# Performance work log

Measured on AMD Instinct MI355X. Metric: run time of the kernel, lower is better.

Reference implementation:

```python
import jax, jax.numpy as jnp
import numpy as np

H = 4          # num_heads
K_HOP = 2
EPS = 1e-5


def _ln(x, g, b):
    m = jnp.mean(x, axis=-1, keepdims=True)
    v = jnp.mean((x - m) ** 2, axis=-1, keepdims=True)
    return (x - m) * jax.lax.rsqrt(v + EPS) * g + b


def setup_inputs() -> dict:
    key = jax.random.key(0)
    B, T, N, D = 16, 24, 512, 64
    F = 256
    ks = jax.random.split(key, 16)
    s = 0.02
    inp = {
        'x': jax.random.normal(ks[0], (B, T, N, D), dtype=jnp.float32),
        'adj': jax.random.uniform(ks[1], (N, N), dtype=jnp.float32),
        'Wq': jax.random.normal(ks[2], (D, D), dtype=jnp.float32) * s,
        'bq': jnp.zeros((D,), jnp.float32),
        'Wk': jax.random.normal(ks[3], (D, D), dtype=jnp.float32) * s,
        'bk': jnp.zeros((D,), jnp.float32),
        'Wv': jax.random.normal(ks[4], (D, D), dtype=jnp.float32) * s,
        'bv': jnp.zeros((D,), jnp.float32),
        'Wo': jax.random.normal(ks[5], (D, D), dtype=jnp.float32) * s,
        'bo': jnp.zeros((D,), jnp.float32),
        'gcW': jax.random.normal(ks[6], (K_HOP + 1, D, D), dtype=jnp.float32) * s,
        'gcb': jnp.zeros((K_HOP + 1, D), jnp.float32),
        'W1': jax.random.normal(ks[7], (D, F), dtype=jnp.float32) * s,
        'b1': jnp.zeros((F,), jnp.float32),
        'W2': jax.random.normal(ks[8], (F, D), dtype=jnp.float32) * s,
        'b2': jnp.zeros((D,), jnp.float32),
        'g_t': jnp.ones((D,), jnp.float32), 'b_t': jnp.zeros((D,), jnp.float32),
        'g_g': jnp.ones((D,), jnp.float32), 'b_g': jnp.zeros((D,), jnp.float32),
        'g_f': jnp.ones((D,), jnp.float32), 'b_f': jnp.zeros((D,), jnp.float32),
    }
    return inp


def _forward(x, adj, Wq, bq, Wk, bk, Wv, bv, Wo, bo, gcW, gcb,
             W1, b1, W2, b2, g_t, b_t, g_g, b_g, g_f, b_f):
    B, T, N, D = x.shape
    hd = D // H
    scale = hd ** -0.5

    # ---- temporal multi-head attention (per node, along T) ----
    def heads(y):
        return y.reshape(B, T, N, H, hd)
    q = heads(x @ Wq + bq)
    k = heads(x @ Wk + bk)
    v = heads(x @ Wv + bv)
    scores = jnp.einsum('bqnhd,bknhd->bnhqk', q, k) * scale  # [B,N,H,T,T]
    attn = jax.nn.softmax(scores, axis=-1)
    att = jnp.einsum('bnhqk,bknhd->bqnhd', attn, v).reshape(B, T, N, D)
    att = att @ Wo + bo
    h = _ln(x + att, g_t, b_t)

    # ---- K-hop graph convolution: sum_k A_hat^k X W_k ----
    A = adj + jnp.eye(N, dtype=adj.dtype)
    deg = A.sum(-1)
    dinv = jnp.clip(deg, 1e-12, None) ** -0.5
    Ahat = dinv[:, None] * A * dinv[None, :]  # [N,N], shared across B*T
    prop = h
    gout = prop @ gcW[0] + gcb[0]
    for kk in range(1, K_HOP + 1):
        prop = jnp.einsum('mn,btnd->btmd', Ahat, prop)
        gout = gout + prop @ gcW[kk] + gcb[kk]
    h = _ln(h + gout, g_g, b_g)

    # ---- FFN (exact GELU, as torch default) ----
    f = jax.nn.gelu(h @ W1 + b1, approximate=False) @ W2 + b2
    return _ln(h + f, g_f, b_f)


def reference(x, adj, Wq, bq, Wk, bk, Wv, bv, Wo, bo, gcW, gcb,
              W1, b1, W2, b2, g_t, b_t, g_g, b_g, g_f, b_f):
    return _forward(x, adj, Wq, bq, Wk, bk, Wv, bv, Wo, bo, gcW, gcb,
                    W1, b1, W2, b2, g_t, b_t, g_g, b_g, g_f, b_f)
```

## Files before the change

kernel.cpp:

```cpp
#include <hip/hip_runtime.h>
#include <hip/hip_bf16.h>
#include <math.h>

typedef __hip_bfloat16 bf16;
typedef unsigned short ushort_t;

__device__ __forceinline__ float us2f(ushort_t u){
  union { unsigned u; float f; } v; v.u = ((unsigned)u) << 16; return v.f;
}
__device__ __forceinline__ ushort_t f2us(float f){
  union { __bf16 b; ushort_t u; } v; v.b = (__bf16)f; return v.u;
}

__device__ __forceinline__ float gelu_f(float x){
  float y = x * fmaf(0.0356774081f, x*x, 0.7978845608f);
  float e = __expf(-2.0f*y);
  return x * __builtin_amdgcn_rcpf(1.0f + e);
}

#define B_ 16
#define T_ 24
#define N_ 512
#define D_ 64
#define F_ 256

typedef __attribute__((ext_vector_type(8)))  short  frag8;
typedef __attribute__((ext_vector_type(16))) float  accv16;

__device__ __forceinline__ float wave_sum(float v){
#pragma unroll
  for (int off = 32; off > 0; off >>= 1) v += __shfl_xor(v, off, 64);
  return v;
}

__global__ __launch_bounds__(64) void k_dinv(const float* __restrict__ adj,
                                             float* __restrict__ dinv){
  int m = blockIdx.x;
  float s = 0.f;
  for (int n = threadIdx.x; n < N_; n += 64) s += adj[m*N_ + n];
  s = wave_sum(s);
  if (threadIdx.x == 0){
    float deg = s + 1.0f;
    dinv[m] = rsqrtf(fmaxf(deg, 1e-12f));
  }
}

__global__ __launch_bounds__(256) void k_ahat(const float* __restrict__ adj,
                                              const float* __restrict__ dinv,
                                              ushort_t* __restrict__ AhatB,
                                              ushort_t* __restrict__ AhatBT){
  int idx = blockIdx.x*256 + threadIdx.x;
  int m = idx >> 9, n = idx & (N_-1);
  float a = adj[idx] + (m == n ? 1.f : 0.f);
  ushort_t v = f2us(dinv[m]*a*dinv[n]);
  AhatB[idx] = v;
  AhatBT[n*N_ + m] = v;
}

__global__ __launch_bounds__(256, 4) void k_ah2(
    const ushort_t* __restrict__ A1,
    const ushort_t* __restrict__ A1T,
    ushort_t* __restrict__ A2)
{
  __shared__ __align__(16) ushort_t Ab[64][72];
  __shared__ __align__(16) ushort_t Bb[64][72];
  __shared__ __align__(16) ushort_t Yt[64][72];
  int tid  = threadIdx.x;
  int lane = tid & 63, w = tid >> 6;
  int mw = (w >> 1) * 32, nw = (w & 1) * 32;
  int l31 = lane & 31, lh = lane >> 5;
  int m0 = blockIdx.x * 64, n0 = blockIdx.y * 64;
  int ar = tid >> 3, ac8 = (tid & 7) * 8;

  accv16 acc = {};
  for (int k0 = 0; k0 < N_; k0 += 64){
#pragma unroll
    for (int g = 0; g < 2; g++){
      int rr = ar + g*32;
      *(uint4*)&Ab[rr][ac8] = *(const uint4*)&A1 [(size_t)(m0 + rr)*N_ + k0 + ac8];
      *(uint4*)&Bb[rr][ac8] = *(const uint4*)&A1T[(size_t)(n0 + rr)*N_ + k0 + ac8];
    }
    __syncthreads();
#pragma unroll
    for (int kk = 0; kk < 64; kk += 16){
      frag8 af = *(const frag8*)&Ab[mw + l31][kk + lh*8];
      frag8 bf = *(const frag8*)&Bb[nw + l31][kk + lh*8];
      acc = __builtin_amdgcn_mfma_f32_32x32x16_bf16(af, bf, acc, 0, 0, 0);
    }
    __syncthreads();
  }
#pragma unroll
  for (int r = 0; r < 16; r++){
    int row = mw + (r & 3) + 8*(r >> 2) + 4*lh;
    Yt[row][nw + l31] = f2us(acc[r]);
  }
  __syncthreads();
#pragma unroll
  for (int g = 0; g < 2; g++){
    int rr = ar + g*32;
    *(uint4*)&A2[(size_t)(m0 + rr)*N_ + n0 + ac8] = *(const uint4*)&Yt[rr][ac8];
  }
}

__global__ __launch_bounds__(256) void k_wprep(
    const float* __restrict__ W1, const float* __restrict__ W2,
    const float* __restrict__ Wq, const float* __restrict__ Wk,
    const float* __restrict__ Wv, const float* __restrict__ Wo,
    const float* __restrict__ gcW,
    ushort_t* __restrict__ W1t, ushort_t* __restrict__ W2t,
    ushort_t* __restrict__ Wqt, ushort_t* __restrict__ Wkt,
    ushort_t* __restrict__ Wvt, ushort_t* __restrict__ Wot,
    ushort_t* __restrict__ gWt){
  int o = blockIdx.x*256 + threadIdx.x;
  int f = o >> 6, e = o & 63;
  W1t[o] = f2us(W1[e*256 + f]);
  int d = o >> 8, e2 = o & 255;
  W2t[o] = f2us(W2[e2*64 + d]);
  if (o < 4096){
    int dd = o >> 6, ee = o & 63;
    Wqt[o] = f2us(Wq[ee*64 + dd]);
    Wkt[o] = f2us(Wk[ee*64 + dd]);
    Wvt[o] = f2us(Wv[ee*64 + dd]);
    Wot[o] = f2us(Wo[ee*64 + dd]);
    gWt[o]        = f2us(gcW[       ee*64 + dd]);
    gWt[4096 + o] = f2us(gcW[4096 + ee*64 + dd]);
    gWt[8192 + o] = f2us(gcW[8192 + ee*64 + dd]);
  }
}

__global__ __launch_bounds__(256, 4) void k_attn_m(
    const float* __restrict__ x,
    const ushort_t* __restrict__ Wqt, const float* __restrict__ bq,
    const ushort_t* __restrict__ Wkt, const float* __restrict__ bk,
    const ushort_t* __restrict__ Wvt, const float* __restrict__ bv,
    const ushort_t* __restrict__ Wot, const float* __restrict__ bo,
    const float* __restrict__ g_t, const float* __restrict__ b_t,
    float* __restrict__ h1)
{
  __shared__ __align__(16) char smem[28928];
  ushort_t (*xsA)[72] = (ushort_t(*)[72]) smem;
  ushort_t (*qs)[72]  = (ushort_t(*)[72])(smem + 6912);
  ushort_t (*ks)[72]  = (ushort_t(*)[72])(smem + 13824);
  float    (*Os)[65]  = (float(*)[65])   (smem + 6912);
  ushort_t *vsT       = (ushort_t*)(smem + 20736);

  int tid = threadIdx.x;
  int lane = tid & 63, w = tid >> 6;
  int l31 = lane & 31, lh = lane >> 5;
  int mt = (w >> 1) * 32, nt = (w & 1) * 32;
  int b = blockIdx.x >> 8;
  int n0 = (blockIdx.x & 255) * 2;

  {
    uint4 z4 = {0,0,0,0};
#pragma unroll
    for (int i = 0; i < 2; i++)
      *(uint4*)(smem + 20736 + (tid + i*256)*16) = z4;
  }
#pragma unroll
  for (int i = 0; i < 3; i++){
    int idx = tid + i*256;
    int row = idx >> 4, d4 = (idx & 15) * 4;
    int node = row >= 24;
    int t = row - node*24;
    const float4 v = *(const float4*)&x[(((size_t)b*T_ + t)*N_ + n0 + node)*D_ + d4];
    ushort_t tmp[4] = { f2us(v.x), f2us(v.y), f2us(v.z), f2us(v.w) };
    *(unsigned long long*)&xsA[row][d4] = *(unsigned long long*)tmp;
  }
  __syncthreads();

#pragma unroll
  for (int pj = 0; pj < 3; pj++){
    const ushort_t* Wp = (pj==0 ? Wqt : pj==1 ? Wkt : Wvt);
    accv16 a = {};
#pragma unroll
    for (int kk = 0; kk < 64; kk += 16){
      frag8 af = *(const frag8*)&xsA[mt + l31][kk + lh*8];
      frag8 bf = *(const frag8*)&Wp[(size_t)(nt + l31)*64 + kk + lh*8];
      a = __builtin_amdgcn_mfma_f32_32x32x16_bf16(af, bf, a, 0, 0, 0);
    }
    float bias = (pj==0 ? bq : pj==1 ? bk : bv)[nt + l31];
    if (pj < 2){
      ushort_t (*dst)[72] = (pj==0 ? qs : ks);
#pragma unroll
      for (int r = 0; r < 16; r++){
        int row = mt + (r & 3) + 8*(r >> 2) + 4*lh;
        if (row < 48) dst[row][nt + l31] = f2us(a[r] + bias);
      }
    } else {
      int cl = nt + l31;
#pragma unroll
      for (int r = 0; r < 16; r++){
        int row = mt + (r & 3) + 8*(r >> 2) + 4*lh;
        if (row < 48){
          int node = (row >= 24);
          int t2 = row - node*24;
          int Rr = node*64 + cl;
          vsT[Rr*32 + (((t2 >> 3) ^ ((Rr >> 1) & 3)) << 3) + (t2 & 7)] = f2us(a[r] + bias);
        }
      }
    }
  }
  __syncthreads();

  int vs_s = (l31 >> 1) & 3;
#pragma unroll
  for (int gi = 0; gi < 2; gi++){
    int g = w*2 + gi;
    int node = g >> 2, hh = g & 3;
    accv16 s = {};
    frag8 kf = *(const frag8*)&ks[node*24 + l31][hh*16 + lh*8];
    frag8 qf = *(const frag8*)&qs[node*24 + l31][hh*16 + lh*8];
    s = __builtin_amdgcn_mfma_f32_32x32x16_bf16(kf, qf, s, 0, 0, 0);
    float e[12]; float sm = 0.f;
#pragma unroll
    for (int r = 0; r < 12; r++){ e[r] = __expf(s[r]*0.25f); sm += e[r]; }
    sm += __shfl_xor(sm, 32, 64);
    float rinv = 1.0f / sm;
    union { unsigned long long q; ushort_t u[4]; } a0, a1, a2;
#pragma unroll
    for (int j = 0; j < 4; j++){
      a0.u[j] = f2us(e[j]   * rinv);
      a1.u[j] = f2us(e[4+j] * rinv);
      a2.u[j] = f2us(e[8+j] * rinv);
    }
    unsigned long long send1 = lh ? a0.q : a1.q;
    unsigned long long r1 = __shfl_xor(send1, 32, 64);
    unsigned long long r2 = __shfl_xor(a2.q, 32, 64);
    union { frag8 f; unsigned long long q[2]; } f0, f1;
    f0.q[0] = lh ? r1   : a0.q;
    f0.q[1] = lh ? a1.q : r1;
    f1.q[0] = lh ? 0ULL : a2.q;
    f1.q[1] = lh ? 0ULL : r2;
    int vrow = node*64 + hh*16 + (l31 & 15);
    const ushort_t* vb = &vsT[vrow*32];
    frag8 bf0 = *(const frag8*)&vb[((0 + lh) ^ vs_s) << 3];
    frag8 bf1 = *(const frag8*)&vb[((2 + lh) ^ vs_s) << 3];
    accv16 acc = {};
    acc = __builtin_amdgcn_mfma_f32_32x32x16_bf16(f0.f, bf0, acc, 0, 0, 0);
    acc = __builtin_amdgcn_mfma_f32_32x32x16_bf16(f1.f, bf1, acc, 0, 0, 0);
    if (l31 < 16){
#pragma unroll
      for (int r = 0; r < 12; r++){
        int row = (r & 3) + 8*(r >> 2) + 4*lh;
        xsA[node*24 + row][hh*16 + l31] = f2us(acc[r]);
      }
    }
  }
  __syncthreads();

  accv16 ao = {};
#pragma unroll
  for (int kk = 0; kk < 64; kk += 16){
    frag8 af = *(const frag8*)&xsA[mt + l31][kk + lh*8];
    frag8 bf = *(const frag8*)&Wot[(size_t)(nt + l31)*64 + kk + lh*8];
    ao = __builtin_amdgcn_mfma_f32_32x32x16_bf16(af, bf, ao, 0, 0, 0);
  }
  {
    float bov = bo[nt + l31];
#pragma unroll
    for (int r = 0; r < 16; r++){
      int row = mt + (r & 3) + 8*(r >> 2) + 4*lh;
      if (row < 48) Os[row][nt + l31] = ao[r] + bov;
    }
  }
  __syncthreads();
  {
    float gv = g_t[lane], bvv = b_t[lane];
#pragma unroll
    for (int i = 0; i < 12; i++){
      int row = w + i*4;
      int node = row >= 24;
      int t = row - node*24;
      size_t gaddr = (((size_t)b*T_ + t)*N_ + n0 + node)*D_ + lane;
      float v = Os[row][lane] + x[gaddr];
      float m = wave_sum(v) * (1.f/64.f);
      float df = v - m;
      float var = wave_sum(df*df) * (1.f/64.f);
      h1[gaddr] = df * rsqrtf(var + 1e-5f) * gv + bvv;
    }
  }
}

__global__ __launch_bounds__(256, 8) void k_hT(const float* __restrict__ h,
                                               ushort_t* __restrict__ hT){
  __shared__ __align__(16) ushort_t tb[64][76];
  int tid = threadIdx.x;
  int n0 = (blockIdx.x & 7) * 64;
  size_t bt = blockIdx.x >> 3;
  const float* src = h + (bt*N_ + n0)*D_;
#pragma unroll
  for (int i = 0; i < 4; i++){
    int q = tid + i*256;
    int row = q >> 4, d4 = (q & 15)*4;
    float4 v = *(const float4*)&src[(size_t)q*4];
    ushort_t tmp[4] = { f2us(v.x), f2us(v.y), f2us(v.z), f2us(v.w) };
    *(unsigned long long*)&tb[row][d4] = *(unsigned long long*)tmp;
  }
  __syncthreads();
  int d = tid >> 2, nseg = (tid & 3)*16;
  ushort_t tmp[16];
#pragma unroll
  for (int j = 0; j < 16; j++){
    int jj = (j + ((d & 7) << 1)) & 15;
    tmp[jj] = tb[nseg + jj][d];
  }
  ushort_t* dst = hT + (bt*D_ + d)*N_ + n0 + nseg;
  *(uint4*)&dst[0] = *(uint4*)&tmp[0];
  *(uint4*)&dst[8] = *(uint4*)&tmp[8];
}

__global__ __launch_bounds__(256, 4) void k_gconv(
    const ushort_t* __restrict__ A1,
    const ushort_t* __restrict__ A2,
    const ushort_t* __restrict__ XT,
    const ushort_t* __restrict__ gW1t,
    const ushort_t* __restrict__ gW2t,
    ushort_t* __restrict__ G)
{
  __shared__ __align__(16) ushort_t Ab1[64][72];
  __shared__ __align__(16) ushort_t Ab2[64][72];
  __shared__ __align__(16) ushort_t Xb[64][72];
  int tid  = threadIdx.x;
  int lane = tid & 63, w = tid >> 6;
  int mw = (w >> 1) * 32, nw = (w & 1) * 32;
  int l31 = lane & 31, lh = lane >> 5;
  int m0 = blockIdx.x * 64;
  size_t slice = (size_t)blockIdx.y * (N_ * D_);
  const ushort_t* Xg = XT + slice;
  int ar = tid >> 3, ac8 = (tid & 7) * 8;

  accv16 acc1 = {}, acc2 = {};
  for (int k0 = 0; k0 < N_; k0 += 64){
#pragma unroll
    for (int g = 0; g < 2; g++){
      int rr = ar + g*32;
      *(uint4*)&Ab1[rr][ac8] = *(const uint4*)&A1[(size_t)(m0 + rr)*N_ + k0 + ac8];
      *(uint4*)&Ab2[rr][ac8] = *(const uint4*)&A2[(size_t)(m0 + rr)*N_ + k0 + ac8];
      *(uint4*)&Xb [rr][ac8] = *(const uint4*)&Xg[(size_t)rr*N_ + k0 + ac8];
    }
    __syncthreads();
#pragma unroll
    for (int kk = 0; kk < 64; kk += 16){
      frag8 bf  = *(const frag8*)&Xb [nw + l31][kk + lh*8];
      frag8 af1 = *(const frag8*)&Ab1[mw + l31][kk + lh*8];
      frag8 af2 = *(const frag8*)&Ab2[mw + l31][kk + lh*8];
      acc1 = __builtin_amdgcn_mfma_f32_32x32x16_bf16(af1, bf, acc1, 0, 0, 0);
      acc2 = __builtin_amdgcn_mfma_f32_32x32x16_bf16(af2, bf, acc2, 0, 0, 0);
    }
    __syncthreads();
  }

#pragma unroll
  for (int r = 0; r < 16; r++){
    int row = mw + (r & 3) + 8*(r >> 2) + 4*lh;
    Ab2[row][nw + l31] = f2us(acc1[r]);
    Ab1[row][nw + l31] = f2us(acc2[r]);
  }
  __syncthreads();

  accv16 ag = {};
#pragma unroll
  for (int kk = 0; kk < 64; kk += 16){
    frag8 a1f = *(const frag8*)&Ab2[mw + l31][kk + lh*8];
    frag8 b1f = *(const frag8*)&gW1t[(size_t)(nw + l31)*64 + kk + lh*8];
    ag = __builtin_amdgcn_mfma_f32_32x32x16_bf16(a1f, b1f, ag, 0, 0, 0);
  }
#pragma unroll
  for (int kk = 0; kk < 64; kk += 16){
    frag8 a2f = *(const frag8*)&Ab1[mw + l31][kk + lh*8];
    frag8 b2f = *(const frag8*)&gW2t[(size_t)(nw + l31)*64 + kk + lh*8];
    ag = __builtin_amdgcn_mfma_f32_32x32x16_bf16(a2f, b2f, ag, 0, 0, 0);
  }
#pragma unroll
  for (int r = 0; r < 16; r++){
    int row = mw + (r & 3) + 8*(r >> 2) + 4*lh;
    Xb[row][nw + l31] = f2us(ag[r]);
  }
  __syncthreads();
#pragma unroll
  for (int g = 0; g < 2; g++){
    int rr = ar + g*32;
    *(uint4*)&G[slice + (size_t)(m0 + rr)*D_ + ac8] = *(const uint4*)&Xb[rr][ac8];
  }
}

__global__ __launch_bounds__(256, 4) void k_cffn(
  const ushort_t* __restrict__ g12,
  const ushort_t* __restrict__ gW0t,
  const float* __restrict__ gcb,
  const float* __restrict__ g_g, const float* __restrict__ b_g,
  const ushort_t* __restrict__ W1t, const ushort_t* __restrict__ W2t,
  const float* __restrict__ b1, const float* __restrict__ b2,
  const float* __restrict__ g_f, const float* __restrict__ b_f,
  float* __restrict__ h)
{
  __shared__ __align__(16) char smem[26624];
  ushort_t (*hsA)[72] = (ushort_t(*)[72]) smem;
  ushort_t (*Uc)[136] = (ushort_t(*)[136])(smem + 9216);
  float    (*Sf)[68]  = (float(*)[68])    (smem + 9216);
  float    (*Os)[68]  = (float(*)[68])    (smem + 9216);

  int tid = threadIdx.x;
  int lane = tid & 63, w = tid >> 6;
  int l31 = lane & 31, lh = lane >> 5;
  size_t tok0 = (size_t)blockIdx.x * 64;

#pragma unroll
  for (int i = 0; i < 4; i++){
    int q = tid + i*256;
    int row = q >> 4, d4 = (q & 15) * 4;
    float4 v = *(const float4*)&h[tok0*64 + (size_t)q*4];
    ushort_t tmp[4] = { f2us(v.x), f2us(v.y), f2us(v.z), f2us(v.w) };
    *(unsigned long long*)&hsA[row][d4] = *(unsigned long long*)tmp;
  }
  __syncthreads();

  {
    int mg = (w >> 1) * 32, ng = (w & 1) * 32;
    accv16 ag = {};
#pragma unroll
    for (int kk = 0; kk < 64; kk += 16){
      frag8 af = *(const frag8*)&hsA[mg + l31][kk + lh*8];
      frag8 bf = *(const frag8*)&gW0t[(size_t)(ng + l31)*64 + kk + lh*8];
      ag = __builtin_amdgcn_mfma_f32_32x32x16_bf16(af, bf, ag, 0, 0, 0);
    }
    int col = ng + l31;
    float bs = gcb[col] + gcb[64 + col] + gcb[128 + col];
#pragma unroll
    for (int r = 0; r < 16; r++){
      int row = mg + (r & 3) + 8*(r >> 2) + 4*lh;
      size_t ga = (tok0 + row)*64 + col;
      Sf[row][col] = ag[r] + h[ga] + us2f(g12[ga]) + bs;
    }
  }
  __syncthreads();

  int rrow = tid >> 2, seg = (tid & 3) * 16;
  float h2r[16];
  {
    float vb[16]; float s1 = 0.f;
#pragma unroll
    for (int j4 = 0; j4 < 4; j4++){
      float4 v = *(const float4*)&Sf[rrow][seg + j4*4];
      vb[j4*4+0] = v.x; vb[j4*4+1] = v.y; vb[j4*4+2] = v.z; vb[j4*4+3] = v.w;
      s1 += v.x + v.y + v.z + v.w;
    }
    s1 += __shfl_xor(s1, 1, 64); s1 += __shfl_xor(s1, 2, 64);
    float m = s1 * (1.f/64.f);
    float s2 = 0.f;
#pragma unroll
    for (int j = 0; j < 16; j++){ vb[j] -= m; s2 += vb[j]*vb[j]; }
    s2 += __shfl_xor(s2, 1, 64); s2 += __shfl_xor(s2, 2, 64);
    float rstd = rsqrtf(s2 * (1.f/64.f) + 1e-5f);
    ushort_t tmp[16];
#pragma unroll
    for (int j4 = 0; j4 < 4; j4++){
      float4 gv = *(const float4*)&g_g[seg + j4*4];
      float4 bv = *(const float4*)&b_g[seg + j4*4];
      h2r[j4*4+0] = vb[j4*4+0]*rstd*gv.x + bv.x;
      h2r[j4*4+1] = vb[j4*4+1]*rstd*gv.y + bv.y;
      h2r[j4*4+2] = vb[j4*4+2]*rstd*gv.z + bv.z;
      h2r[j4*4+3] = vb[j4*4+3]*rstd*gv.w + bv.w;
    }
#pragma unroll
    for (int j = 0; j < 16; j++) tmp[j] = f2us(h2r[j]);
    *(uint4*)&hsA[rrow][seg]     = *(uint4*)&tmp[0];
    *(uint4*)&hsA[rrow][seg + 8] = *(uint4*)&tmp[8];
  }
  __syncthreads();

  int mw1 = (w & 1) * 32, nA = (w >> 1) * 32;
  int mw2 = (w >> 1) * 32, dw = (w & 1) * 32;
  accv16 acc2 = {};
#pragma unroll
  for (int f0 = 0; f0 < F_; f0 += 128){
    if (f0) __syncthreads();
    accv16 accA = {}, accB = {};
#pragma unroll
    for (int kk = 0; kk < 64; kk += 16){
      frag8 af  = *(const frag8*)&hsA[mw1 + l31][kk + lh*8];
      frag8 b0  = *(const frag8*)&W1t[(size_t)(f0 + nA + l31)*64 + kk + lh*8];
      frag8 b1f = *(const frag8*)&W1t[(size_t)(f0 + nA + 64 + l31)*64 + kk + lh*8];
      accA = __builtin_amdgcn_mfma_f32_32x32x16_bf16(af, b0,  accA, 0, 0, 0);
      accB = __builtin_amdgcn_mfma_f32_32x32x16_bf16(af, b1f, accB, 0, 0, 0);
    }
    {
      float bA = b1[f0 + nA + l31];
      float bB = b1[f0 + nA + 64 + l31];
#pragma unroll
      for (int r = 0; r < 16; r++){
        int row = mw1 + (r & 3) + 8*(r >> 2) + 4*lh;
        Uc[row][nA + l31]      = f2us(gelu_f(accA[r] + bA));
        Uc[row][nA + 64 + l31] = f2us(gelu_f(accB[r] + bB));
      }
    }
    __syncthreads();
#pragma unroll
    for (int kk = 0; kk < 128; kk += 16){
      frag8 af = *(const frag8*)&Uc[mw2 + l31][kk + lh*8];
      frag8 bf = *(const frag8*)&W2t[(size_t)(dw + l31)*256 + f0 + kk + lh*8];
      acc2 = __builtin_amdgcn_mfma_f32_32x32x16_bf16(af, bf, acc2, 0, 0, 0);
    }
  }
  __syncthreads();
  {
    float b2v = b2[dw + l31];
#pragma unroll
    for (int r = 0; r < 16; r++){
      int row = mw2 + (r & 3) + 8*(r >> 2) + 4*lh;
      Os[row][dw + l31] = acc2[r] + b2v;
    }
  }
  __syncthreads();

  {
    float vb[16]; float s1 = 0.f;
#pragma unroll
    for (int j4 = 0; j4 < 4; j4++){
      float4 v = *(const float4*)&Os[rrow][seg + j4*4];
      vb[j4*4+0] = v.x + h2r[j4*4+0];
      vb[j4*4+1] = v.y + h2r[j4*4+1];
      vb[j4*4+2] = v.z + h2r[j4*4+2];
      vb[j4*4+3] = v.w + h2r[j4*4+3];
      s1 += vb[j4*4+0] + vb[j4*4+1] + vb[j4*4+2] + vb[j4*4+3];
    }
    s1 += __shfl_xor(s1, 1, 64); s1 += __shfl_xor(s1, 2, 64);
    float m = s1 * (1.f/64.f);
    float s2 = 0.f;
#pragma unroll
    for (int j = 0; j < 16; j++){ vb[j] -= m; s2 += vb[j]*vb[j]; }
    s2 += __shfl_xor(s2, 1, 64); s2 += __shfl_xor(s2, 2, 64);
    float rstd = rsqrtf(s2 * (1.f/64.f) + 1e-5f);
#pragma unroll
    for (int j4 = 0; j4 < 4; j4++){
      float4 gv = *(const float4*)&g_f[seg + j4*4];
      float4 bv = *(const float4*)&b_f[seg + j4*4];
      float4 st;
      st.x = vb[j4*4+0]*rstd*gv.x + bv.x;
      st.y = vb[j4*4+1]*rstd*gv.y + bv.y;
      st.z = vb[j4*4+2]*rstd*gv.z + bv.z;
      st.w = vb[j4*4+3]*rstd*gv.w + bv.w;
      *(float4*)&h[(tok0 + rrow)*64 + seg + j4*4] = st;
    }
  }
}

extern "C" void kernel_launch(void* const* d_in, const int* in_sizes, int n_in,
                              void* d_out, int out_size, void* d_ws, size_t ws_size,
                              hipStream_t stream)
{
  const float* x   = (const float*)d_in[0];
  const float* adj = (const float*)d_in[1];
  const float* Wq  = (const float*)d_in[2];
  const float* bq  = (const float*)d_in[3];
  const float* Wk  = (const float*)d_in[4];
  const float* bk  = (const float*)d_in[5];
  const float* Wv  = (const float*)d_in[6];
  const float* bv  = (const float*)d_in[7];
  const float* Wo  = (const float*)d_in[8];
  const float* bo  = (const float*)d_in[9];
  const float* gcW = (const float*)d_in[10];
  const float* gcb = (const float*)d_in[11];
  const float* W1  = (const float*)d_in[12];
  const float* b1  = (const float*)d_in[13];
  const float* W2  = (const float*)d_in[14];
  const float* b2  = (const float*)d_in[15];
  const float* g_t = (const float*)d_in[16];
  const float* b_t = (const float*)d_in[17];
  const float* g_g = (const float*)d_in[18];
  const float* b_g = (const float*)d_in[19];
  const float* g_f = (const float*)d_in[20];
  const float* b_f = (const float*)d_in[21];

  const size_t MD = (size_t)B_*T_*N_*D_;
  const size_t NN = (size_t)N_*N_;
  float* dinv = (float*)d_ws;
  ushort_t* AhatB  = (ushort_t*)(dinv + 512);
  ushort_t* AhatBT = AhatB + NN;
  ushort_t* AhatB2 = AhatBT + NN;
  ushort_t* g12 = AhatB2 + NN;
  ushort_t* hT  = g12 + MD;
  ushort_t* W1t = hT + MD;
  ushort_t* W2t = W1t + 256*64;
  ushort_t* Wqt = W2t + 64*256;
  ushort_t* Wkt = Wqt + 4096;
  ushort_t* Wvt = Wkt + 4096;
  ushort_t* Wot = Wvt + 4096;
  ushort_t* gWt = Wot + 4096;
  float* h = (float*)d_out;

  k_dinv<<<N_, 64, 0, stream>>>(adj, dinv);
  k_ahat<<<(N_*N_)/256, 256, 0, stream>>>(adj, dinv, AhatB, AhatBT);
  k_wprep<<<64, 256, 0, stream>>>(W1, W2, Wq, Wk, Wv, Wo, gcW,
                                  W1t, W2t, Wqt, Wkt, Wvt, Wot, gWt);
  k_ah2<<<dim3(8, 8), 256, 0, stream>>>(AhatB, AhatBT, AhatB2);
  k_attn_m<<<B_*N_/2, 256, 0, stream>>>(x, Wqt,bq, Wkt,bk, Wvt,bv, Wot,bo, g_t,b_t, h);
  k_hT<<<B_*T_*8, 256, 0, stream>>>(h, hT);
  k_gconv<<<dim3(N_/64, B_*T_), 256, 0, stream>>>(AhatB, AhatB2, hT,
                                                  gWt + 4096, gWt + 8192, g12);
  k_cffn<<<(int)(MD/D_/64), 256, 0, stream>>>(g12, gWt, gcb, g_g, b_g,
                                              W1t, W2t, b1, b2, g_f, b_f, h);
}
```

Before: 370.5 us.

## Fuse graph convolution and FFN into one kernel, dropping the g12 intermediate

Merges the K-hop graph convolution kernel with the residual/LayerNorm/FFN kernel so each block computes A·X, A²·X, all three hop projections and the FFN for a 64-token tile in one pass. This removes the bf16 g12 intermediate write and re-read (about 25 MB each way) and one kernel launch. Shared memory is reused across phases and grows slightly (27 KB), and the kernel does more work per block, which may affect occupancy. The hop-1 and hop-2 projections are also no longer rounded to bf16 before being summed.

```diff
diff --git a/kernel.cpp b/kernel.cpp
--- a/kernel.cpp
+++ b/kernel.cpp
@@ -310,128 +310,101 @@
   *(uint4*)&dst[8] = *(uint4*)&tmp[8];
 }
 
-__global__ __launch_bounds__(256, 4) void k_gconv(
+__global__ __launch_bounds__(256, 4) void k_gcffn(
     const ushort_t* __restrict__ A1,
     const ushort_t* __restrict__ A2,
     const ushort_t* __restrict__ XT,
-    const ushort_t* __restrict__ gW1t,
-    const ushort_t* __restrict__ gW2t,
-    ushort_t* __restrict__ G)
+    const ushort_t* __restrict__ gWt,
+    const float* __restrict__ gcb,
+    const float* __restrict__ g_g, const float* __restrict__ b_g,
+    const ushort_t* __restrict__ W1t, const ushort_t* __restrict__ W2t,
+    const float* __restrict__ b1, const float* __restrict__ b2,
+    const float* __restrict__ g_f, const float* __restrict__ b_f,
+    float* __restrict__ h)
 {
-  __shared__ __align__(16) ushort_t Ab1[64][72];
-  __shared__ __align__(16) ushort_t Ab2[64][72];
-  __shared__ __align__(16) ushort_t Xb[64][72];
-  int tid  = threadIdx.x;
-  int lane = tid & 63, w = tid >> 6;
-  int mw = (w >> 1) * 32, nw = (w & 1) * 32;
-  int l31 = lane & 31, lh = lane >> 5;
-  int m0 = blockIdx.x * 64;
-  size_t slice = (size_t)blockIdx.y * (N_ * D_);
-  const ushort_t* Xg = XT + slice;
-  int ar = tid >> 3, ac8 = (tid & 7) * 8;
-
-  accv16 acc1 = {}, acc2 = {};
-  for (int k0 = 0; k0 < N_; k0 += 64){
-#pragma unroll
-    for (int g = 0; g < 2; g++){
-      int rr = ar + g*32;
-      *(uint4*)&Ab1[rr][ac8] = *(const uint4*)&A1[(size_t)(m0 + rr)*N_ + k0 + ac8];
-      *(uint4*)&Ab2[rr][ac8] = *(const uint4*)&A2[(size_t)(m0 + rr)*N_ + k0 + ac8];
-      *(uint4*)&Xb [rr][ac8] = *(const uint4*)&Xg[(size_t)rr*N_ + k0 + ac8];
-    }
-    __syncthreads();
-#pragma unroll
-    for (int kk = 0; kk < 64; kk += 16){
-      frag8 bf  = *(const frag8*)&Xb [nw + l31][kk + lh*8];
-      frag8 af1 = *(const frag8*)&Ab1[mw + l31][kk + lh*8];
-      frag8 af2 = *(const frag8*)&Ab2[mw + l31][kk + lh*8];
-      acc1 = __builtin_amdgcn_mfma_f32_32x32x16_bf16(af1, bf, acc1, 0, 0, 0);
-      acc2 = __builtin_amdgcn_mfma_f32_32x32x16_bf16(af2, bf, acc2, 0, 0, 0);
-    }
-    __syncthreads();
-  }
-
-#pragma unroll
-  for (int r = 0; r < 16; r++){
-    int row = mw + (r & 3) + 8*(r >> 2) + 4*lh;
-    Ab2[row][nw + l31] = f2us(acc1[r]);
-    Ab1[row][nw + l31] = f2us(acc2[r]);
-  }
-  __syncthreads();
-
-  accv16 ag = {};
-#pragma unroll
-  for (int kk = 0; kk < 64; kk += 16){
-    frag8 a1f = *(const frag8*)&Ab2[mw + l31][kk + lh*8];
-    frag8 b1f = *(const frag8*)&gW1t[(size_t)(nw + l31)*64 + kk + lh*8];
-    ag = __builtin_amdgcn_mfma_f32_32x32x16_bf16(a1f, b1f, ag, 0, 0, 0);
-  }
-#pragma unroll
-  for (int kk = 0; kk < 64; kk += 16){
-    frag8 a2f = *(const frag8*)&Ab1[mw + l31][kk + lh*8];
-    frag8 b2f = *(const frag8*)&gW2t[(size_t)(nw + l31)*64 + kk + lh*8];
-    ag = __builtin_amdgcn_mfma_f32_32x32x16_bf16(a2f, b2f, ag, 0, 0, 0);
-  }
-#pragma unroll
-  for (int r = 0; r < 16; r++){
-    int row = mw + (r & 3) + 8*(r >> 2) + 4*lh;
-    Xb[row][nw + l31] = f2us(ag[r]);
-  }
-  __syncthreads();
-#pragma unroll
-  for (int g = 0; g < 2; g++){
-    int rr = ar + g*32;
-    *(uint4*)&G[slice + (size_t)(m0 + rr)*D_ + ac8] = *(const uint4*)&Xb[rr][ac8];
-  }
-}
-
-__global__ __launch_bounds__(256, 4) void k_cffn(
-  const ushort_t* __restrict__ g12,
-  const ushort_t* __restrict__ gW0t,
-  const float* __restrict__ gcb,
-  const float* __restrict__ g_g, const float* __restrict__ b_g,
-  const ushort_t* __restrict__ W1t, const ushort_t* __restrict__ W2t,
-  const float* __restrict__ b1, const float* __restrict__ b2,
-  const float* __restrict__ g_f, const float* __restrict__ b_f,
-  float* __restrict__ h)
-{
-  __shared__ __align__(16) char smem[26624];
-  ushort_t (*hsA)[72] = (ushort_t(*)[72]) smem;
-  ushort_t (*Uc)[136] = (ushort_t(*)[136])(smem + 9216);
-  float    (*Sf)[68]  = (float(*)[68])    (smem + 9216);
-  float    (*Os)[68]  = (float(*)[68])    (smem + 9216);
+  __shared__ __align__(16) char smem[27648];
+  ushort_t (*R0)[72]  = (ushort_t(*)[72]) smem;
+  ushort_t (*R1)[72]  = (ushort_t(*)[72])(smem +  9216);
+  ushort_t (*hsA)[72] = (ushort_t(*)[72])(smem + 18432);
+  float    (*Sf)[68]  = (float(*)[68])    smem;
+  ushort_t (*Uc)[136] = (ushort_t(*)[136])smem;
+  float    (*Os)[68]  = (float(*)[68])    smem;
 
   int tid = threadIdx.x;
   int lane = tid & 63, w = tid >> 6;
   int l31 = lane & 31, lh = lane >> 5;
-  size_t tok0 = (size_t)blockIdx.x * 64;
-
+  int mw = (w >> 1) * 32, nw = (w & 1) * 32;
+  int m0 = blockIdx.x * 64;
+  size_t bt = blockIdx.y;
+  const ushort_t* Xg = XT + bt * (N_ * D_);
+  size_t tokbase = bt * N_ + m0;
+  int ar = tid >> 3, ac8 = (tid & 7) * 8;
+
+  accv16 acc1 = {}, acc2 = {};
+  for (int k0 = 0; k0 < N_; k0 += 64){
+#pragma unroll
+    for (int g = 0; g < 2; g++){
+      int rr = ar + g*32;
+      *(uint4*)&R0 [rr][ac8] = *(const uint4*)&A1[(size_t)(m0 + rr)*N_ + k0 + ac8];
+      *(uint4*)&R1 [rr][ac8] = *(const uint4*)&A2[(size_t)(m0 + rr)*N_ + k0 + ac8];
+      *(uint4*)&hsA[rr][ac8] = *(const uint4*)&Xg[(size_t)rr*N_ + k0 + ac8];
+    }
+    __syncthreads();
+#pragma unroll
+    for (int kk = 0; kk < 64; kk += 16){
+      frag8 bf  = *(const frag8*)&hsA[nw + l31][kk + lh*8];
+      frag8 af1 = *(const frag8*)&R0 [mw + l31][kk + lh*8];
+      frag8 af2 = *(const frag8*)&R1 [mw + l31][kk + lh*8];
+      acc1 = __builtin_amdgcn_mfma_f32_32x32x16_bf16(af1, bf, acc1, 0, 0, 0);
+      acc2 = __builtin_amdgcn_mfma_f32_32x32x16_bf16(af2, bf, acc2, 0, 0, 0);
+    }
+    __syncthreads();
+  }
+
+#pragma unroll
+  for (int r = 0; r < 16; r++){
+    int row = mw + (r & 3) + 8*(r >> 2) + 4*lh;
+    R1[row][nw + l31] = f2us(acc1[r]);
+    R0[row][nw + l31] = f2us(acc2[r]);
+  }
 #pragma unroll
   for (int i = 0; i < 4; i++){
     int q = tid + i*256;
     int row = q >> 4, d4 = (q & 15) * 4;
-    float4 v = *(const float4*)&h[tok0*64 + (size_t)q*4];
+    float4 v = *(const float4*)&h[tokbase*64 + (size_t)q*4];
     ushort_t tmp[4] = { f2us(v.x), f2us(v.y), f2us(v.z), f2us(v.w) };
     *(unsigned long long*)&hsA[row][d4] = *(unsigned long long*)tmp;
   }
   __syncthreads();
 
-  {
-    int mg = (w >> 1) * 32, ng = (w & 1) * 32;
-    accv16 ag = {};
-#pragma unroll
-    for (int kk = 0; kk < 64; kk += 16){
-      frag8 af = *(const frag8*)&hsA[mg + l31][kk + lh*8];
-      frag8 bf = *(const frag8*)&gW0t[(size_t)(ng + l31)*64 + kk + lh*8];
-      ag = __builtin_amdgcn_mfma_f32_32x32x16_bf16(af, bf, ag, 0, 0, 0);
-    }
-    int col = ng + l31;
+  accv16 ag = {};
+#pragma unroll
+  for (int kk = 0; kk < 64; kk += 16){
+    frag8 a0f = *(const frag8*)&hsA[mw + l31][kk + lh*8];
+    frag8 b0f = *(const frag8*)&gWt[(size_t)(nw + l31)*64 + kk + lh*8];
+    ag = __builtin_amdgcn_mfma_f32_32x32x16_bf16(a0f, b0f, ag, 0, 0, 0);
+  }
+#pragma unroll
+  for (int kk = 0; kk < 64; kk += 16){
+    frag8 a1f = *(const frag8*)&R1[mw + l31][kk + lh*8];
+    frag8 b1f = *(const frag8*)&gWt[4096 + (size_t)(nw + l31)*64 + kk + lh*8];
+    ag = __builtin_amdgcn_mfma_f32_32x32x16_bf16(a1f, b1f, ag, 0, 0, 0);
+  }
+#pragma unroll
+  for (int kk = 0; kk < 64; kk += 16){
+    frag8 a2f = *(const frag8*)&R0[mw + l31][kk + lh*8];
+    frag8 b2f = *(const frag8*)&gWt[8192 + (size_t)(nw + l31)*64 + kk + lh*8];
+    ag = __builtin_amdgcn_mfma_f32_32x32x16_bf16(a2f, b2f, ag, 0, 0, 0);
+  }
+  __syncthreads();
+
+  {
+    int col = nw + l31;
     float bs = gcb[col] + gcb[64 + col] + gcb[128 + col];
 #pragma unroll
     for (int r = 0; r < 16; r++){
-      int row = mg + (r & 3) + 8*(r >> 2) + 4*lh;
-      size_t ga = (tok0 + row)*64 + col;
-      Sf[row][col] = ag[r] + h[ga] + us2f(g12[ga]) + bs;
+      int row = mw + (r & 3) + 8*(r >> 2) + 4*lh;
+      Sf[row][col] = ag[r] + h[(tokbase + row)*64 + col] + bs;
     }
   }
   __syncthreads();
@@ -472,7 +445,7 @@
 
   int mw1 = (w & 1) * 32, nA = (w >> 1) * 32;
   int mw2 = (w >> 1) * 32, dw = (w & 1) * 32;
-  accv16 acc2 = {};
+  accv16 accO = {};
 #pragma unroll
   for (int f0 = 0; f0 < F_; f0 += 128){
     if (f0) __syncthreads();
@@ -500,7 +473,7 @@
     for (int kk = 0; kk < 128; kk += 16){
       frag8 af = *(const frag8*)&Uc[mw2 + l31][kk + lh*8];
       frag8 bf = *(const frag8*)&W2t[(size_t)(dw + l31)*256 + f0 + kk + lh*8];
-      acc2 = __builtin_amdgcn_mfma_f32_32x32x16_bf16(af, bf, acc2, 0, 0, 0);
+      accO = __builtin_amdgcn_mfma_f32_32x32x16_bf16(af, bf, accO, 0, 0, 0);
     }
   }
   __syncthreads();
@@ -509,7 +482,7 @@
 #pragma unroll
     for (int r = 0; r < 16; r++){
       int row = mw2 + (r & 3) + 8*(r >> 2) + 4*lh;
-      Os[row][dw + l31] = acc2[r] + b2v;
+      Os[row][dw + l31] = accO[r] + b2v;
     }
   }
   __syncthreads();
@@ -541,7 +514,7 @@
       st.y = vb[j4*4+1]*rstd*gv.y + bv.y;
       st.z = vb[j4*4+2]*rstd*gv.z + bv.z;
       st.w = vb[j4*4+3]*rstd*gv.w + bv.w;
-      *(float4*)&h[(tok0 + rrow)*64 + seg + j4*4] = st;
+      *(float4*)&h[(tokbase + rrow)*64 + seg + j4*4] = st;
     }
   }
 }
@@ -579,8 +552,7 @@
   ushort_t* AhatB  = (ushort_t*)(dinv + 512);
   ushort_t* AhatBT = AhatB + NN;
   ushort_t* AhatB2 = AhatBT + NN;
-  ushort_t* g12 = AhatB2 + NN;
-  ushort_t* hT  = g12 + MD;
+  ushort_t* hT  = AhatB2 + NN;
   ushort_t* W1t = hT + MD;
   ushort_t* W2t = W1t + 256*64;
   ushort_t* Wqt = W2t + 64*256;
@@ -597,8 +569,7 @@
   k_ah2<<<dim3(8, 8), 256, 0, stream>>>(AhatB, AhatBT, AhatB2);
   k_attn_m<<<B_*N_/2, 256, 0, stream>>>(x, Wqt,bq, Wkt,bk, Wvt,bv, Wot,bo, g_t,b_t, h);
   k_hT<<<B_*T_*8, 256, 0, stream>>>(h, hT);
-  k_gconv<<<dim3(N_/64, B_*T_), 256, 0, stream>>>(AhatB, AhatB2, hT,
-                                                  gWt + 4096, gWt + 8192, g12);
-  k_cffn<<<(int)(MD/D_/64), 256, 0, stream>>>(g12, gWt, gcb, g_g, b_g,
-                                              W1t, W2t, b1, b2, g_f, b_f, h);
-}
+  k_gcffn<<<dim3(N_/64, B_*T_), 256, 0, stream>>>(AhatB, AhatB2, hT, gWt,
+                                                  gcb, g_g, b_g,
+                                                  W1t, W2t, b1, b2, g_f, b_f, h);
+}
```

New measurement: 346.8 us. 1.07x faster.
